# Kernel tuning notes

Hardware: AMD Instinct MI355X
Metric: run time of the kernel (lower is better)

The kernel has to match this reference:

```python
import jax, jax.numpy as jnp
import numpy as np

DIM = 512; NHEAD = 8; DHEAD = 64; INNER = NHEAD * DHEAD
CTX = 1024; NOCT = int(np.ceil(np.log2(CTX))) + 1  # 11
B = 8; SEQ = 256; MEM = 768


def positional_encoding(ctx, num_oct):
    # matches Attention.positional_encoding on coords=arange(ctx).view(ctx,1),
    # start_octave = 1 - num_oct
    coords = jnp.arange(ctx, dtype=jnp.float32)[:, None, None]        # (ctx,1,1)
    octaves = jnp.arange(1 - num_oct, 1, dtype=jnp.float32)           # (num_oct,)
    mult = (2.0 ** octaves) * np.pi
    scaled = (coords * mult).reshape(ctx, num_oct)                    # (ctx, num_oct)
    return jnp.concatenate([jnp.sin(scaled), jnp.cos(scaled)], axis=-1)  # (ctx, 2*num_oct)


def get_shifts(mem, seq, ctx):
    coords = jnp.arange(mem + seq - 1, -1, -1) - (seq - 1)            # (mem+seq,)
    shifts = coords[None, :] + jnp.arange(seq)[:, None]               # (seq, mem+seq)
    oob = (shifts < 0) | (shifts > ctx - 1)
    bias = jnp.where(oob, -jnp.inf, 0.0).astype(jnp.float32)
    return jnp.clip(shifts, 0, ctx - 1), bias


def setup_inputs() -> dict:
    key = jax.random.key(0)
    ks = jax.random.split(key, 8)
    s = 0.02
    return {
        "x": jax.random.normal(ks[0], (B, SEQ, DIM), jnp.float32),
        "memory": jax.random.normal(ks[1], (B, MEM, DIM), jnp.float32),
        "W_qkv": jax.random.normal(ks[2], (DIM, 3 * INNER), jnp.float32) * s,
        "W_rel": jax.random.normal(ks[3], (2 * NOCT, INNER), jnp.float32) * s,
        "W_out": jax.random.normal(ks[4], (INNER, DIM), jnp.float32) * s,
        "b_out": jnp.zeros((DIM,), jnp.float32),
        "u_emb": jax.random.normal(ks[5], (DHEAD,), jnp.float32),
        "v_emb": jax.random.normal(ks[6], (DHEAD,), jnp.float32),
    }


def reference(x, memory, W_qkv, W_rel, W_out, b_out, u_emb, v_emb):
    b, seq, _ = x.shape
    mem = memory.shape[1]
    total = mem + seq
    scale = DHEAD ** -0.5

    shifts, bias = get_shifts(mem, seq, CTX)                          # (seq,total) each
    R = positional_encoding(CTX, NOCT)                                # (CTX, 2*NOCT)
    kr = (R @ W_rel)[shifts].reshape(seq, total, NHEAD, DHEAD)        # n m h d

    qkv = jnp.concatenate([memory, x], axis=1) @ W_qkv                # (b,total,3*INNER)
    q, k, v = jnp.split(qkv, 3, axis=-1)

    def heads(t):
        return t.reshape(b, total, NHEAD, DHEAD).transpose(0, 2, 1, 3)  # b h m d

    q = heads(q)[:, :, mem:]                                          # b h n d (queries only over x)
    k = heads(k)
    v = heads(v)

    term_a = jnp.einsum('bhnd,bhmd->bhnm', q, k)
    term_b = jnp.einsum('bhnd,nmhd->bhnm', q, kr)
    term_c = jnp.einsum('d,bhmd->bhm', u_emb, k)[:, :, None, :]        # broadcast over n
    term_d = jnp.einsum('d,nmhd->hnm', v_emb, kr)[None]                # broadcast over b

    dots = (term_a + term_b + term_c + term_d) * scale + bias          # banded -inf mask
    attn = jax.nn.softmax(dots, axis=-1)                               # dropout p=0 -> identity
    out = jnp.einsum('bhnm,bhmd->bnhd', attn, v).reshape(b, seq, INNER)
    return out @ W_out + b_out
```

## Files before the change

### kernel.cpp

```cpp
#include <hip/hip_runtime.h>
#include <hip/hip_bf16.h>
#include <math.h>

typedef unsigned short u16;
typedef unsigned int u32;
typedef __attribute__((ext_vector_type(8))) short short8;
typedef __attribute__((ext_vector_type(4))) float floatx4;

constexpr int kB     = 8;
constexpr int kSEQ   = 256;
constexpr int kMEM   = 768;
constexpr int kTOTAL = 1024;

__device__ __forceinline__ float bf2f(u16 u) {
  return __uint_as_float(((u32)u) << 16);
}
__device__ __forceinline__ u16 f2bf(float f) {
  __hip_bfloat16 h = __float2bfloat16(f);
  return *reinterpret_cast<u16*>(&h);
}
__device__ __forceinline__ void gload_lds16(const u16* g, u16* l) {
  __builtin_amdgcn_global_load_lds(
      (__attribute__((address_space(1))) const unsigned int*)g,
      (__attribute__((address_space(3))) unsigned int*)l, 16, 0, 0);
}

__device__ __forceinline__ void wtconv_body(
    const float* __restrict__ W, u16* __restrict__ Wt, int K, int N,
    int n0, int k0, int tid, float (*tile)[65])
{
  int r = tid >> 4, c4 = (tid & 15) * 4;
#pragma unroll
  for (int v = 0; v < 4; v++) {
    float4 w4 = *(const float4*)(W + (size_t)(k0 + v * 16 + r) * N + n0 + c4);
    tile[v * 16 + r][c4 + 0] = w4.x;
    tile[v * 16 + r][c4 + 1] = w4.y;
    tile[v * 16 + r][c4 + 2] = w4.z;
    tile[v * 16 + r][c4 + 3] = w4.w;
  }
  __syncthreads();
#pragma unroll
  for (int v = 0; v < 4; v++) {
    int rn = v * 16 + r;
    ushort4 o;
    o.x = f2bf(tile[c4 + 0][rn]);
    o.y = f2bf(tile[c4 + 1][rn]);
    o.z = f2bf(tile[c4 + 2][rn]);
    o.w = f2bf(tile[c4 + 3][rn]);
    *(ushort4*)(Wt + (size_t)(n0 + rn) * K + k0 + c4) = o;
  }
}

__global__ __launch_bounds__(256) void prep_kernel(
    const float* __restrict__ x, const float* __restrict__ memf,
    const float* __restrict__ W_qkv, const float* __restrict__ W_out,
    const float* __restrict__ W_rel, const float* __restrict__ v_emb,
    const float* __restrict__ u_emb,
    u16* __restrict__ Xb, u16* __restrict__ WqkvT, u16* __restrict__ WoutT,
    u16* __restrict__ Rrel_bf, float* __restrict__ vR)
{
  __shared__ float tile[64][65];
  __shared__ float pe[22];
  __shared__ float prod[512];
  int bid = blockIdx.x;
  int t = threadIdx.x;
  if (bid < 1024) {
    int s = bid;
    if (t < 22) {
      int o = (t < 11) ? t : (t - 11);
      float mult = ldexpf(3.14159265358979323846f, o - 10);
      float ang = (float)s * mult;
      pe[t] = (t < 11) ? sinf(ang) : cosf(ang);
    }
    __syncthreads();
#pragma unroll
    for (int c = 0; c < 2; c++) {
      int j = t + c * 256;
      float acc = 0.f;
#pragma unroll
      for (int o = 0; o < 22; ++o) acc += pe[o] * W_rel[o * 512 + j];
      u16 rbf = f2bf(acc);
      Rrel_bf[(size_t)s * 512 + j] = rbf;
      prod[j] = acc * v_emb[j & 63] - bf2f(rbf) * u_emb[j & 63];
    }
    __syncthreads();
    if (t < 8) {
      float a = 0.f;
#pragma unroll 8
      for (int d = 0; d < 64; d++) a += prod[t * 64 + d];
      vR[t * 1024 + s] = a * 0.125f;
    }
  } else if (bid < 3072) {
    int idx = (bid - 1024) * 256 + t;
    int row = idx >> 6, c8 = idx & 63;
    int b = row >> 10, pos = row & 1023;
    const float* src = (pos < kMEM)
        ? memf + (size_t)(b * kMEM + pos) * 512
        : x    + (size_t)(b * kSEQ + pos - kMEM) * 512;
    const float4* s4 = (const float4*)(src + c8 * 8);
    float4 a = s4[0], bb = s4[1];
    u16 tmp[8] = {f2bf(a.x),  f2bf(a.y),  f2bf(a.z),  f2bf(a.w),
                  f2bf(bb.x), f2bf(bb.y), f2bf(bb.z), f2bf(bb.w)};
    *(uint4*)(Xb + (size_t)row * 512 + c8 * 8) = *(uint4*)tmp;
  } else if (bid < 3264) {
    int r = bid - 3072;
    wtconv_body(W_qkv, WqkvT, 512, 1536, (r % 24) * 64, (r / 24) * 64, t, tile);
  } else {
    int r = bid - 3264;
    wtconv_body(W_out, WoutT, 512, 512, (r % 8) * 64, (r / 8) * 64, t, tile);
  }
}

__global__ __launch_bounds__(256) void gemm_qkv(
    const u16* __restrict__ A, const u16* __restrict__ Bt,
    u16* __restrict__ Cbf, const float* __restrict__ uq)
{
  __shared__ u16 As[64 * 64];
  __shared__ u16 Bs[128 * 64];
  int tid = threadIdx.x;
  int id = blockIdx.y * gridDim.x + blockIdx.x;
  int bm = (id % 128) * 64, bn = (id / 128) * 128;
  if (bn < 512 && ((bm >> 6) & 15) < 12) return;
  int ln = tid & 15, quad = (tid >> 4) & 3, w = tid >> 6;
  int moff = (w >> 1) * 32, noff = (w & 1) * 64;
  int l7 = ln & 7;
  floatx4 acc[2][4];
#pragma unroll
  for (int mi = 0; mi < 2; mi++)
#pragma unroll
    for (int ni = 0; ni < 4; ni++) acc[mi][ni] = (floatx4){0.f, 0.f, 0.f, 0.f};

  int srow[4], sgch[4];
#pragma unroll
  for (int v = 0; v < 4; v++) {
    int f = v * 256 + tid;
    srow[v] = f >> 3;
    sgch[v] = (f & 7) ^ ((f >> 3) & 7);
  }

  for (int ks = 0; ks < 8; ks++) {
    int k0 = ks * 64;
#pragma unroll
    for (int v = 0; v < 2; v++)
      gload_lds16(A + (size_t)(bm + srow[v]) * 512 + k0 + sgch[v] * 8,
                  &As[(v * 256 + tid) * 8]);
#pragma unroll
    for (int v = 0; v < 4; v++)
      gload_lds16(Bt + (size_t)(bn + srow[v]) * 512 + k0 + sgch[v] * 8,
                  &Bs[(v * 256 + tid) * 8]);
    __syncthreads();
#pragma unroll
    for (int kb = 0; kb < 2; kb++) {
      short8 af[2], bfr[4];
#pragma unroll
      for (int mi = 0; mi < 2; mi++) {
        int row = moff + mi * 16 + ln;
        af[mi] = *(const short8*)&As[row * 64 + (((quad + 4 * kb) ^ l7) << 3)];
      }
#pragma unroll
      for (int ni = 0; ni < 4; ni++) {
        int row = noff + ni * 16 + ln;
        bfr[ni] = *(const short8*)&Bs[row * 64 + (((quad + 4 * kb) ^ l7) << 3)];
      }
#pragma unroll
      for (int mi = 0; mi < 2; mi++)
#pragma unroll
        for (int ni = 0; ni < 4; ni++)
          acc[mi][ni] = __builtin_amdgcn_mfma_f32_16x16x32_bf16(
              af[mi], bfr[ni], acc[mi][ni], 0, 0, 0);
    }
    __syncthreads();
  }

  int r0 = bm + moff + quad * 4;
#pragma unroll
  for (int ni = 0; ni < 4; ni++) {
    int col = bn + noff + ni * 16 + ln;
    bool isq = col < 512;
    float scale = isq ? 0.125f : 1.f;
    float uadd = isq ? uq[col & 63] : 0.f;
#pragma unroll
    for (int mi = 0; mi < 2; mi++) {
#pragma unroll
      for (int r = 0; r < 4; r++) {
        int row = r0 + mi * 16 + r;
        Cbf[(size_t)row * 1536 + col] = f2bf((acc[mi][ni][r] + uadd) * scale);
      }
    }
  }
}

__global__ __launch_bounds__(256) void attn_mfma(
    const u16* __restrict__ qkv_bf, const u16* __restrict__ Rrel_bf,
    const float* __restrict__ vR,
    u16* __restrict__ Opart, float* __restrict__ lbuf)
{
  constexpr int LD = 72;
  __shared__ u16 Vt[2][64 * LD];
  __shared__ u16 Ps[64 * LD];

  int h = blockIdx.x;
  int nt = blockIdx.y >> 2, p = blockIdx.y & 3;
  int b = blockIdx.z;
  int n0 = nt * 64, bh = b * 8 + h;
  int tid = threadIdx.x;
  int w = tid >> 6, lane = tid & 63;
  int l15 = lane & 15, quad = lane >> 4, q8 = quad * 8;

  int sr0 = tid >> 3, sc8 = tid & 7;
  int sr1 = (256 + tid) >> 3;
  int vg0 = ((sr0 >> 3) ^ sc8) * 8 + (sr0 & 7);
  int vg1 = ((sr1 >> 3) ^ sc8) * 8 + (sr1 & 7);

  const u16* kpart = qkv_bf + (size_t)(b * kTOTAL) * 1536 + 512 + h * 64;
  const float* vRh = vR + h * 1024;
  int s_base_w = kMEM + n0 + 16 * w;

  const u16* qrow = qkv_bf + (size_t)(b * kTOTAL + kMEM + n0 + 16 * w + l15) * 1536 + h * 64;
  short8 qf0 = *(const short8*)(qrow + q8);
  short8 qf1 = *(const short8*)(qrow + 32 + q8);

  int bidx[4];
#pragma unroll
  for (int r = 0; r < 4; r++) {
    int il = 4 * quad + r;
    bidx[r] = ((quad << 4) | ((il + 15 - l15) & 15)) << 2;
  }

  auto load_V = [&](int mtu, int mtv, uint4 (&vr)[4]) {
    const u16* va = kpart + (size_t)mtu * 64 * 1536 + 512;
    const u16* vb = kpart + (size_t)mtv * 64 * 1536 + 512;
    vr[0] = *(const uint4*)(va + (size_t)sr0 * 1536 + sc8 * 8);
    vr[1] = *(const uint4*)(va + (size_t)sr1 * 1536 + sc8 * 8);
    vr[2] = *(const uint4*)(vb + (size_t)sr0 * 1536 + sc8 * 8);
    vr[3] = *(const uint4*)(vb + (size_t)sr1 * 1536 + sc8 * 8);
  };
  auto write_V = [&](uint4 (&vr)[4], u16* bu, u16* bv) {
    const u16* c0 = (const u16*)&vr[0];
    const u16* c1 = (const u16*)&vr[1];
    const u16* c2 = (const u16*)&vr[2];
    const u16* c3 = (const u16*)&vr[3];
#pragma unroll
    for (int i = 0; i < 8; i++) {
      bu[(sc8 * 8 + i) * LD + vg0] = c0[i];
      bu[(sc8 * 8 + i) * LD + vg1] = c1[i];
      bv[(sc8 * 8 + i) * LD + vg0] = c2[i];
      bv[(sc8 * 8 + i) * LD + vg1] = c3[i];
    }
  };
  auto load_K = [&](int mt, short8 (&k0)[4], short8 (&k1)[4]) {
#pragma unroll
    for (int ni = 0; ni < 4; ni++) {
      const u16* kr = kpart + (size_t)(mt * 64 + 16 * ni + l15) * 1536;
      k0[ni] = *(const short8*)(kr + q8);
      k1[ni] = *(const short8*)(kr + 32 + q8);
    }
  };
  auto load_R = [&](int sb, short8 (&r0)[5], short8 (&r1)[5], float (&vc)[5]) {
#pragma unroll
    for (int ct = 0; ct < 5; ct++) {
      int s = sb - 63 + 16 * ct + l15;
      s = min(max(s, 0), 1023);
      const u16* rr = Rrel_bf + (size_t)s * 512 + h * 64;
      r0[ct] = *(const short8*)(rr + q8);
      r1[ct] = *(const short8*)(rr + 32 + q8);
      vc[ct] = vRh[s];
    }
  };

  floatx4 o_acc[4];
  float l_i[4];
#pragma unroll
  for (int r = 0; r < 4; r++) l_i[r] = 0.f;
#pragma unroll
  for (int nd = 0; nd < 4; nd++) o_acc[nd] = (floatx4){0.f, 0.f, 0.f, 0.f};

  auto do_T = [&](short8 (&rb0)[5], short8 (&rb1)[5], float (&vRc)[5],
                  float (&tf)[5][4]) {
#pragma unroll
    for (int ct = 0; ct < 5; ct++) {
      floatx4 t = (floatx4){0.f, 0.f, 0.f, 0.f};
      t = __builtin_amdgcn_mfma_f32_16x16x32_bf16(qf0, rb0[ct], t, 0, 0, 0);
      t = __builtin_amdgcn_mfma_f32_16x16x32_bf16(qf1, rb1[ct], t, 0, 0, 0);
#pragma unroll
      for (int r = 0; r < 4; r++) tf[ct][r] = t[r] + vRc[ct];
    }
  };
  auto do_tsh = [&](float (&tf)[5][4], float (&tsh)[4][4]) {
#pragma unroll
    for (int ni = 0; ni < 4; ni++) {
#pragma unroll
      for (int r = 0; r < 4; r++) {
        int il = 4 * quad + r;
        float tv = (l15 < il) ? tf[4 - ni][r] : tf[3 - ni][r];
        tsh[ni][r] = __int_as_float(
            __builtin_amdgcn_ds_bpermute(bidx[r], __float_as_int(tv)));
      }
    }
  };
  auto do_QK = [&](short8 (&kb0)[4], short8 (&kb1)[4], floatx4 (&sa)[4]) {
#pragma unroll
    for (int ni = 0; ni < 4; ni++) {
      floatx4 s4 = (floatx4){0.f, 0.f, 0.f, 0.f};
      s4 = __builtin_amdgcn_mfma_f32_16x16x32_bf16(qf0, kb0[ni], s4, 0, 0, 0);
      s4 = __builtin_amdgcn_mfma_f32_16x16x32_bf16(qf1, kb1[ni], s4, 0, 0, 0);
      sa[ni] = s4;
    }
  };
  auto do_logits = [&](floatx4 (&sa)[4], float (&tsh)[4][4], int sb) {
#pragma unroll
    for (int ni = 0; ni < 4; ni++) {
#pragma unroll
      for (int r = 0; r < 4; r++) {
        int il = 4 * quad + r;
        float val = sa[ni][r] + tsh[ni][r];
        if ((16 * ni + l15) > (sb + il)) val = -1e30f;
        float e = __expf(val);
        l_i[r] += e;
        int prow = 16 * w + il;
        Ps[prow * LD + (l15 & 7) + (((2 * ni + (l15 >> 3)) ^ (prow >> 3)) << 3)] =
            f2bf(e);
      }
    }
  };
  auto do_PV = [&](const u16* VtX) {
    int rowq = 16 * w + l15, rr3q = rowq >> 3;
    short8 pa0 = *(const short8*)&Ps[rowq * LD + ((quad ^ rr3q) << 3)];
    short8 pa1 = *(const short8*)&Ps[rowq * LD + (((quad + 4) ^ rr3q) << 3)];
#pragma unroll
    for (int nd = 0; nd < 4; nd++) {
      int rowv = 16 * nd + l15, rr3v = rowv >> 3;
      short8 vb0 = *(const short8*)&VtX[rowv * LD + ((quad ^ rr3v) << 3)];
      short8 vb1 = *(const short8*)&VtX[rowv * LD + (((quad + 4) ^ rr3v) << 3)];
      o_acc[nd] = __builtin_amdgcn_mfma_f32_16x16x32_bf16(pa0, vb0, o_acc[nd], 0, 0, 0);
      o_acc[nd] = __builtin_amdgcn_mfma_f32_16x16x32_bf16(pa1, vb1, o_acc[nd], 0, 0, 0);
    }
  };

  short8 rbU0[5], rbU1[5];
  float vRcU[5];
  uint4 vsl[4];
  {
    uint4 v0[4];
    load_V(p, p + 4, v0);
    write_V(v0, Vt[0], Vt[1]);
  }
  load_V(p + 8, p + 12, vsl);
  load_R(s_base_w - 64 * p, rbU0, rbU1, vRcU);
  __syncthreads();

#pragma unroll
  for (int g = 0; g < 2; g++) {
    int mtU = p + 8 * g, mtV = mtU + 4;
    int sbU = s_base_w - 64 * mtU, sbV = s_base_w - 64 * mtV;

    if (g == 1) write_V(vsl, Vt[0], Vt[1]);

    short8 kbU0[4], kbU1[4];
    load_K(mtU, kbU0, kbU1);

    float tfU[5][4], tshU[4][4];
    do_T(rbU0, rbU1, vRcU, tfU);
    do_tsh(tfU, tshU);

    short8 rbV0[5], rbV1[5];
    float vRcV[5];
    load_R(sbV, rbV0, rbV1, vRcV);

    floatx4 saU[4];
    do_QK(kbU0, kbU1, saU);
    do_logits(saU, tshU, sbU);

    short8 kbV0[4], kbV1[4];
    load_K(mtV, kbV0, kbV1);
    if (g == 0)
      load_R(s_base_w - 64 * (p + 8), rbU0, rbU1, vRcU);

    float tfV[5][4], tshV[4][4];
    do_T(rbV0, rbV1, vRcV, tfV);
    do_tsh(tfV, tshV);

    if (g == 1) __syncthreads();
    do_PV(Vt[0]);

    floatx4 saV[4];
    do_QK(kbV0, kbV1, saV);
    do_logits(saV, tshV, sbV);
    do_PV(Vt[1]);

    if (g == 0) __syncthreads();
  }

  int pbase = (p * 64 + bh) * 256;
#pragma unroll
  for (int r = 0; r < 4; r++) {
    float l = l_i[r];
#pragma unroll
    for (int off = 1; off < 16; off <<= 1)
      l += __shfl_xor(l, off, 64);
    int n = n0 + 16 * w + 4 * quad + r;
    u16* orow = Opart + ((size_t)(pbase + n) << 6) + l15;
#pragma unroll
    for (int nd = 0; nd < 4; nd++)
      orow[16 * nd] = f2bf(o_acc[nd][r]);
    if (l15 == 0) lbuf[pbase + n] = l;
  }
}

__global__ __launch_bounds__(256) void gemm_out_fused(
    const u16* __restrict__ Opart, const float* __restrict__ lbuf,
    const u16* __restrict__ Bt, float* __restrict__ Cf,
    const float* __restrict__ bias)
{
  __shared__ u16 As[64 * 64];
  __shared__ u16 Bs[32 * 64];
  __shared__ float invl[64][8];
  int tid = threadIdx.x;
  int id = blockIdx.y * gridDim.x + blockIdx.x;
  int bm = (id % 32) * 64, bn = (id / 32) * 32;
  int ln = tid & 15, quad = (tid >> 4) & 3, w = tid >> 6;
  int l7 = ln & 7;

  int sr = tid >> 2, dq = (tid & 3) * 16;
  int growq = bm + sr, bq = growq >> 8, nq = growq & 255;
  int cg0 = dq >> 3;
  u16* dst0 = &As[sr * 64 + ((cg0 ^ (sr & 7)) << 3)];
  u16* dst1 = &As[sr * 64 + (((cg0 + 1) ^ (sr & 7)) << 3)];

  auto load_O = [&](int ks, uint4 (&pf)[8]) {
    const u16* ob = Opart + (((size_t)(bq * 8 + ks) << 8) + nq) * 64 + dq;
#pragma unroll
    for (int p = 0; p < 4; p++) {
      const u16* src = ob + ((size_t)p << 20);
      pf[2 * p]     = *(const uint4*)src;
      pf[2 * p + 1] = *(const uint4*)(src + 8);
    }
  };

  int srowB = tid >> 3;
  int sgchB = (tid & 7) ^ ((tid >> 3) & 7);

  uint4 pfA[8], pfB[8];
  load_O(0, pfA);

#pragma unroll
  for (int e = tid; e < 512; e += 256) {
    int r = e >> 3, hh = e & 7;
    int grow = bm + r, b = grow >> 8, n = grow & 255;
    int bh = b * 8 + hh;
    float den = 0.f;
#pragma unroll
    for (int p = 0; p < 4; p++) den += lbuf[((p * 64 + bh) << 8) + n];
    invl[r][hh] = 1.f / den;
  }

  floatx4 acc[2];
#pragma unroll
  for (int ni = 0; ni < 2; ni++) acc[ni] = (floatx4){0.f, 0.f, 0.f, 0.f};

  __syncthreads();

  auto body = [&](int ks, uint4 (&cur)[8], uint4 (&nxt)[8], bool last) {
    gload_lds16(Bt + (size_t)(bn + srowB) * 512 + ks * 64 + sgchB * 8,
                &Bs[tid * 8]);
    if (!last) load_O(ks + 1, nxt);

    {
      float inv = invl[sr][ks];
      float sum[16];
#pragma unroll
      for (int j = 0; j < 16; j++) sum[j] = 0.f;
#pragma unroll
      for (int p = 0; p < 4; p++) {
        const u16* u0 = (const u16*)&cur[2 * p];
        const u16* u1 = (const u16*)&cur[2 * p + 1];
#pragma unroll
        for (int j = 0; j < 8; j++) sum[j] += bf2f(u0[j]);
#pragma unroll
        for (int j = 0; j < 8; j++) sum[8 + j] += bf2f(u1[j]);
      }
      u16 ov[16];
#pragma unroll
      for (int j = 0; j < 16; j++) ov[j] = f2bf(sum[j] * inv);
      *(uint4*)dst0 = *(uint4*)&ov[0];
      *(uint4*)dst1 = *(uint4*)&ov[8];
    }
    __syncthreads();

#pragma unroll
    for (int kb = 0; kb < 2; kb++) {
      int rowA = w * 16 + ln;
      short8 af = *(const short8*)&As[rowA * 64 + (((quad + 4 * kb) ^ l7) << 3)];
      short8 bfr[2];
#pragma unroll
      for (int ni = 0; ni < 2; ni++) {
        int row = ni * 16 + ln;
        bfr[ni] = *(const short8*)&Bs[row * 64 + (((quad + 4 * kb) ^ l7) << 3)];
      }
#pragma unroll
      for (int ni = 0; ni < 2; ni++)
        acc[ni] = __builtin_amdgcn_mfma_f32_16x16x32_bf16(af, bfr[ni], acc[ni], 0, 0, 0);
    }
    __syncthreads();
  };

  body(0, pfA, pfB, false);
  body(1, pfB, pfA, false);
  body(2, pfA, pfB, false);
  body(3, pfB, pfA, false);
  body(4, pfA, pfB, false);
  body(5, pfB, pfA, false);
  body(6, pfA, pfB, false);
  body(7, pfB, pfA, true);

  int r0 = bm + w * 16 + quad * 4;
#pragma unroll
  for (int ni = 0; ni < 2; ni++) {
    int col = bn + ni * 16 + ln;
    float cv = bias[col];
#pragma unroll
    for (int r = 0; r < 4; r++)
      Cf[(size_t)(r0 + r) * 512 + col] = acc[ni][r] + cv;
  }
}

extern "C" void kernel_launch(void* const* d_in, const int* in_sizes, int n_in,
                              void* d_out, int out_size, void* d_ws, size_t ws_size,
                              hipStream_t stream) {
  (void)in_sizes; (void)n_in; (void)out_size; (void)ws_size;
  const float* x      = (const float*)d_in[0];
  const float* memory = (const float*)d_in[1];
  const float* W_qkv  = (const float*)d_in[2];
  const float* W_rel  = (const float*)d_in[3];
  const float* W_out  = (const float*)d_in[4];
  const float* b_out  = (const float*)d_in[5];
  const float* u_emb  = (const float*)d_in[6];
  const float* v_emb  = (const float*)d_in[7];
  float* out = (float*)d_out;

  char* ws = (char*)d_ws;
  u16*   qkv_bf  = (u16*)ws;                         ws += (size_t)12582912 * 2;
  u16*   Xcat_bf = (u16*)ws;                         ws += (size_t)4194304 * 2;
  u16*   Opart   = (u16*)ws;                         ws += (size_t)4194304 * 2;
  float* lbuf    = (float*)ws;                       ws += (size_t)65536 * 4;
  u16*   WqkvT   = (u16*)ws;                         ws += (size_t)786432 * 2;
  u16*   WoutT   = (u16*)ws;                         ws += (size_t)262144 * 2;
  u16*   Rrel_bf = (u16*)ws;                         ws += (size_t)524288 * 2;
  float* vR      = (float*)ws;                       ws += (size_t)8192 * 4;

  prep_kernel<<<3328, 256, 0, stream>>>(
      x, memory, W_qkv, W_out, W_rel, v_emb, u_emb,
      Xcat_bf, WqkvT, WoutT, Rrel_bf, vR);

  gemm_qkv<<<dim3(12, 128), 256, 0, stream>>>(
      Xcat_bf, WqkvT, qkv_bf, u_emb);

  attn_mfma<<<dim3(8, 16, 8), 256, 0, stream>>>(
      qkv_bf, Rrel_bf, vR, Opart, lbuf);

  gemm_out_fused<<<dim3(16, 32), 256, 0, stream>>>(
      Opart, lbuf, WoutT, out, b_out);
}
```

Baseline: 152.4 us.

## Fuse fp32-to-bf16 conversion into the QKV GEMM and merge prep launches

The QKV GEMM now reads fp32 activations and W_qkv directly, converts them to bf16 in registers and writes them into swizzled LDS tiles. This removes the separate Xcat and WqkvT bf16 staging buffers and one kernel launch. The prep work that remains (positional projection and W_out transpose) runs as extra blocks of the same launch. In exchange, the GEMM loads twice as many bytes in fp32, repeats the W_qkv conversion in every M-block, uses scattered 2-byte LDS stores for B, and loses the async global-to-LDS loads.

```diff
diff --git a/kernel.cpp b/kernel.cpp
--- a/kernel.cpp
+++ b/kernel.cpp
@@ -25,57 +25,32 @@
       (__attribute__((address_space(3))) unsigned int*)l, 16, 0, 0);
 }
 
-__device__ __forceinline__ void wtconv_body(
-    const float* __restrict__ W, u16* __restrict__ Wt, int K, int N,
-    int n0, int k0, int tid, float (*tile)[65])
-{
-  int r = tid >> 4, c4 = (tid & 15) * 4;
-#pragma unroll
-  for (int v = 0; v < 4; v++) {
-    float4 w4 = *(const float4*)(W + (size_t)(k0 + v * 16 + r) * N + n0 + c4);
-    tile[v * 16 + r][c4 + 0] = w4.x;
-    tile[v * 16 + r][c4 + 1] = w4.y;
-    tile[v * 16 + r][c4 + 2] = w4.z;
-    tile[v * 16 + r][c4 + 3] = w4.w;
-  }
-  __syncthreads();
-#pragma unroll
-  for (int v = 0; v < 4; v++) {
-    int rn = v * 16 + r;
-    ushort4 o;
-    o.x = f2bf(tile[c4 + 0][rn]);
-    o.y = f2bf(tile[c4 + 1][rn]);
-    o.z = f2bf(tile[c4 + 2][rn]);
-    o.w = f2bf(tile[c4 + 3][rn]);
-    *(ushort4*)(Wt + (size_t)(n0 + rn) * K + k0 + c4) = o;
-  }
-}
-
-__global__ __launch_bounds__(256) void prep_kernel(
+__global__ __launch_bounds__(256) void mega_prep_qkv(
     const float* __restrict__ x, const float* __restrict__ memf,
     const float* __restrict__ W_qkv, const float* __restrict__ W_out,
     const float* __restrict__ W_rel, const float* __restrict__ v_emb,
     const float* __restrict__ u_emb,
-    u16* __restrict__ Xb, u16* __restrict__ WqkvT, u16* __restrict__ WoutT,
+    u16* __restrict__ Cbf, u16* __restrict__ WoutT,
     u16* __restrict__ Rrel_bf, float* __restrict__ vR)
 {
-  __shared__ float tile[64][65];
-  __shared__ float pe[22];
-  __shared__ float prod[512];
+  __shared__ char smem[24576];
   int bid = blockIdx.x;
-  int t = threadIdx.x;
+  int tid = threadIdx.x;
+
   if (bid < 1024) {
+    float* pe   = (float*)smem;
+    float* prod = (float*)(smem + 128);
     int s = bid;
-    if (t < 22) {
-      int o = (t < 11) ? t : (t - 11);
+    if (tid < 22) {
+      int o = (tid < 11) ? tid : (tid - 11);
       float mult = ldexpf(3.14159265358979323846f, o - 10);
       float ang = (float)s * mult;
-      pe[t] = (t < 11) ? sinf(ang) : cosf(ang);
+      pe[tid] = (tid < 11) ? sinf(ang) : cosf(ang);
     }
     __syncthreads();
 #pragma unroll
     for (int c = 0; c < 2; c++) {
-      int j = t + c * 256;
+      int j = tid + c * 256;
       float acc = 0.f;
 #pragma unroll
       for (int o = 0; o < 22; ++o) acc += pe[o] * W_rel[o * 512 + j];
@@ -84,43 +59,47 @@
       prod[j] = acc * v_emb[j & 63] - bf2f(rbf) * u_emb[j & 63];
     }
     __syncthreads();
-    if (t < 8) {
+    if (tid < 8) {
       float a = 0.f;
 #pragma unroll 8
-      for (int d = 0; d < 64; d++) a += prod[t * 64 + d];
-      vR[t * 1024 + s] = a * 0.125f;
-    }
-  } else if (bid < 3072) {
-    int idx = (bid - 1024) * 256 + t;
-    int row = idx >> 6, c8 = idx & 63;
-    int b = row >> 10, pos = row & 1023;
-    const float* src = (pos < kMEM)
-        ? memf + (size_t)(b * kMEM + pos) * 512
-        : x    + (size_t)(b * kSEQ + pos - kMEM) * 512;
-    const float4* s4 = (const float4*)(src + c8 * 8);
-    float4 a = s4[0], bb = s4[1];
-    u16 tmp[8] = {f2bf(a.x),  f2bf(a.y),  f2bf(a.z),  f2bf(a.w),
-                  f2bf(bb.x), f2bf(bb.y), f2bf(bb.z), f2bf(bb.w)};
-    *(uint4*)(Xb + (size_t)row * 512 + c8 * 8) = *(uint4*)tmp;
-  } else if (bid < 3264) {
-    int r = bid - 3072;
-    wtconv_body(W_qkv, WqkvT, 512, 1536, (r % 24) * 64, (r / 24) * 64, t, tile);
-  } else {
-    int r = bid - 3264;
-    wtconv_body(W_out, WoutT, 512, 512, (r % 8) * 64, (r / 8) * 64, t, tile);
-  }
-}
-
-__global__ __launch_bounds__(256) void gemm_qkv(
-    const u16* __restrict__ A, const u16* __restrict__ Bt,
-    u16* __restrict__ Cbf, const float* __restrict__ uq)
-{
-  __shared__ u16 As[64 * 64];
-  __shared__ u16 Bs[128 * 64];
-  int tid = threadIdx.x;
-  int id = blockIdx.y * gridDim.x + blockIdx.x;
-  int bm = (id % 128) * 64, bn = (id / 128) * 128;
+      for (int d = 0; d < 64; d++) a += prod[tid * 64 + d];
+      vR[tid * 1024 + s] = a * 0.125f;
+    }
+    return;
+  }
+
+  if (bid < 1088) {
+    float (*tile)[65] = (float(*)[65])smem;
+    int rr = bid - 1024;
+    int n0 = (rr % 8) * 64, k0 = (rr / 8) * 64;
+    int r = tid >> 4, c4 = (tid & 15) * 4;
+#pragma unroll
+    for (int v = 0; v < 4; v++) {
+      float4 w4 = *(const float4*)(W_out + (size_t)(k0 + v * 16 + r) * 512 + n0 + c4);
+      tile[v * 16 + r][c4 + 0] = w4.x;
+      tile[v * 16 + r][c4 + 1] = w4.y;
+      tile[v * 16 + r][c4 + 2] = w4.z;
+      tile[v * 16 + r][c4 + 3] = w4.w;
+    }
+    __syncthreads();
+#pragma unroll
+    for (int v = 0; v < 4; v++) {
+      int rn = v * 16 + r;
+      ushort4 o;
+      o.x = f2bf(tile[c4 + 0][rn]);
+      o.y = f2bf(tile[c4 + 1][rn]);
+      o.z = f2bf(tile[c4 + 2][rn]);
+      o.w = f2bf(tile[c4 + 3][rn]);
+      *(ushort4*)(WoutT + (size_t)(n0 + rn) * 512 + k0 + c4) = o;
+    }
+    return;
+  }
+
+  int gid = bid - 1088;
+  int bm = (gid % 128) * 64, bn = (gid / 128) * 128;
   if (bn < 512 && ((bm >> 6) & 15) < 12) return;
+  u16* As = (u16*)smem;
+  u16* Bs = (u16*)(smem + 8192);
   int ln = tid & 15, quad = (tid >> 4) & 3, w = tid >> 6;
   int moff = (w >> 1) * 32, noff = (w & 1) * 64;
   int l7 = ln & 7;
@@ -130,24 +109,53 @@
 #pragma unroll
     for (int ni = 0; ni < 4; ni++) acc[mi][ni] = (floatx4){0.f, 0.f, 0.f, 0.f};
 
-  int srow[4], sgch[4];
-#pragma unroll
-  for (int v = 0; v < 4; v++) {
-    int f = v * 256 + tid;
-    srow[v] = f >> 3;
-    sgch[v] = (f & 7) ^ ((f >> 3) & 7);
-  }
-
-  for (int ks = 0; ks < 8; ks++) {
-    int k0 = ks * 64;
-#pragma unroll
-    for (int v = 0; v < 2; v++)
-      gload_lds16(A + (size_t)(bm + srow[v]) * 512 + k0 + sgch[v] * 8,
-                  &As[(v * 256 + tid) * 8]);
-#pragma unroll
-    for (int v = 0; v < 4; v++)
-      gload_lds16(Bt + (size_t)(bn + srow[v]) * 512 + k0 + sgch[v] * 8,
-                  &Bs[(v * 256 + tid) * 8]);
+  int sr = tid >> 2, kc = (tid & 3) * 16;
+  int grow = bm + sr, ab = grow >> 10, pos = grow & 1023;
+  const float* asrc = (pos < kMEM)
+      ? memf + (size_t)(ab * kMEM + pos) * 512
+      : x    + (size_t)(ab * kSEQ + pos - kMEM) * 512;
+  int c0 = (tid & 3) * 2;
+  u16* adst0 = &As[sr * 64 + ((c0 ^ (sr & 7)) << 3)];
+  u16* adst1 = &As[sr * 64 + (((c0 + 1) ^ (sr & 7)) << 3)];
+
+  auto load_A = [&](int ks, float4 (&af)[4]) {
+    const float4* s4 = (const float4*)(asrc + ks * 64 + kc);
+#pragma unroll
+    for (int v = 0; v < 4; v++) af[v] = s4[v];
+  };
+  auto write_A = [&](float4 (&af)[4]) {
+    u16 tmp[16];
+    const float* f = (const float*)af;
+#pragma unroll
+    for (int j = 0; j < 16; j++) tmp[j] = f2bf(f[j]);
+    *(uint4*)adst0 = *(uint4*)&tmp[0];
+    *(uint4*)adst1 = *(uint4*)&tmp[8];
+  };
+
+  float4 pA[4], pB[4];
+  load_A(0, pA);
+
+  auto body = [&](int ks, float4 (&cur)[4], float4 (&nxt)[4], bool last) {
+    float4 bw[8];
+#pragma unroll
+    for (int v = 0; v < 8; v++) {
+      int idx = v * 256 + tid;
+      int kr = idx >> 5, c4 = (idx & 31) * 4;
+      bw[v] = *(const float4*)&W_qkv[(size_t)(ks * 64 + kr) * 1536 + bn + c4];
+    }
+    if (!last) load_A(ks + 1, nxt);
+    write_A(cur);
+#pragma unroll
+    for (int v = 0; v < 8; v++) {
+      int idx = v * 256 + tid;
+      int kr = idx >> 5, c4 = (idx & 31) * 4;
+      const float* f = (const float*)&bw[v];
+#pragma unroll
+      for (int j = 0; j < 4; j++) {
+        int n = c4 + j;
+        Bs[n * 64 + (((kr >> 3) ^ (n & 7)) << 3) + (kr & 7)] = f2bf(f[j]);
+      }
+    }
     __syncthreads();
 #pragma unroll
     for (int kb = 0; kb < 2; kb++) {
@@ -170,7 +178,16 @@
               af[mi], bfr[ni], acc[mi][ni], 0, 0, 0);
     }
     __syncthreads();
-  }
+  };
+
+  body(0, pA, pB, false);
+  body(1, pB, pA, false);
+  body(2, pA, pB, false);
+  body(3, pB, pA, false);
+  body(4, pA, pB, false);
+  body(5, pB, pA, false);
+  body(6, pA, pB, false);
+  body(7, pB, pA, true);
 
   int r0 = bm + moff + quad * 4;
 #pragma unroll
@@ -178,7 +195,7 @@
     int col = bn + noff + ni * 16 + ln;
     bool isq = col < 512;
     float scale = isq ? 0.125f : 1.f;
-    float uadd = isq ? uq[col & 63] : 0.f;
+    float uadd = isq ? u_emb[col & 63] : 0.f;
 #pragma unroll
     for (int mi = 0; mi < 2; mi++) {
 #pragma unroll
@@ -540,20 +557,15 @@
 
   char* ws = (char*)d_ws;
   u16*   qkv_bf  = (u16*)ws;                         ws += (size_t)12582912 * 2;
-  u16*   Xcat_bf = (u16*)ws;                         ws += (size_t)4194304 * 2;
   u16*   Opart   = (u16*)ws;                         ws += (size_t)4194304 * 2;
   float* lbuf    = (float*)ws;                       ws += (size_t)65536 * 4;
-  u16*   WqkvT   = (u16*)ws;                         ws += (size_t)786432 * 2;
   u16*   WoutT   = (u16*)ws;                         ws += (size_t)262144 * 2;
   u16*   Rrel_bf = (u16*)ws;                         ws += (size_t)524288 * 2;
   float* vR      = (float*)ws;                       ws += (size_t)8192 * 4;
 
-  prep_kernel<<<3328, 256, 0, stream>>>(
+  mega_prep_qkv<<<2624, 256, 0, stream>>>(
       x, memory, W_qkv, W_out, W_rel, v_emb, u_emb,
-      Xcat_bf, WqkvT, WoutT, Rrel_bf, vR);
-
-  gemm_qkv<<<dim3(12, 128), 256, 0, stream>>>(
-      Xcat_bf, WqkvT, qkv_bf, u_emb);
+      qkv_bf, WoutT, Rrel_bf, vR);
 
   attn_mfma<<<dim3(8, 16, 8), 256, 0, stream>>>(
       qkv_bf, Rrel_bf, vR, Opart, lbuf);
```

New measurement: 222.7 us. +46.1%, slower.
